# Kernel optimization log

Hardware: AMD Instinct MI355X
Metric: run time of the kernel (lower is better)

The kernel has to match this reference:

```python
import jax, jax.numpy as jnp
import numpy as np

EPS_LOG = 1e-10
DECAY = 0.99
RESET_THRESHOLD = 2


def setup_inputs() -> dict:
    key = jax.random.key(0)
    ks = jax.random.split(key, 8)
    B, C_in, T = 4, 1024, 2048
    K, D = 8192, 256
    N = B * T
    return {
        "z": jax.random.normal(ks[0], (B, C_in, T), dtype=jnp.float32),
        "u": jax.random.uniform(ks[1], (N, K), dtype=jnp.float32),
        "Wi": jax.random.normal(ks[2], (D, C_in), dtype=jnp.float32) * 0.02,
        "bi": jax.random.normal(ks[3], (D,), dtype=jnp.float32) * 0.02,
        "Wo": jax.random.normal(ks[4], (C_in, D), dtype=jnp.float32) * 0.02,
        "bo": jax.random.normal(ks[5], (C_in,), dtype=jnp.float32) * 0.02,
        "embedding": jax.random.normal(ks[6], (K, D), dtype=jnp.float32),
        "cluster_size": jnp.zeros((K,), dtype=jnp.float32),
    }


def reference(z, u, Wi, bi, Wo, bo, embedding, cluster_size):
    B, _, T = z.shape
    K, D = embedding.shape
    N = B * T

    # inproj: Conv1d with kernel_size=1 == pointwise linear over channel dim
    z_e = jnp.einsum('bit,di->bdt', z, Wi) + bi[None, :, None]  # (B, D, T)
    z_d = z_e.transpose(0, 2, 1).reshape(N, D)                   # (b t) d

    # squared-euclidean distances via norm expansion
    dist = ((z_d ** 2).sum(axis=1, keepdims=True)
            - 2.0 * (z_d @ embedding.T)
            + (embedding ** 2).sum(axis=1))                      # (N, K)

    # gumbel noise (training=True), softmax_temp = 1.0
    gumbel = -jnp.log(-jnp.log(u + EPS_LOG) + EPS_LOG)
    logits = -dist + gumbel
    y_soft = jax.nn.softmax(logits, axis=-1)                     # (N, K)

    z_q_flat = y_soft @ embedding                                # (N, D)

    # kl_div(log(avg+eps), uniform target of shape (N,K), reduction='sum')
    avg_probs = y_soft.mean(axis=0)                              # (K,)
    inv_k = 1.0 / K
    kl_loss = N * jnp.sum(inv_k * (jnp.log(inv_k) - jnp.log(avg_probs + EPS_LOG)))

    indices = jnp.argmax(y_soft, axis=1)                         # (N,) int

    z_q = z_q_flat.reshape(B, T, D).transpose(0, 2, 1)           # (B, D, T)
    vq_loss = jnp.mean((z_e - jax.lax.stop_gradient(z_q)) ** 2)

    # outproj: Conv1d kernel_size=1
    out = jnp.einsum('bdt,od->bot', z_q, Wo) + bo[None, :, None]  # (B, C_in, T)

    # box_result: active_num uses cluster_size BEFORE the EMA update
    active_num = (cluster_size > RESET_THRESHOLD).sum().astype(z.dtype)
    counts = jnp.zeros((K,), z.dtype).at[indices].add(1.0)       # one-hot column sums
    probs = counts / N                                           # == mean(one_hot, axis=0)
    perplexity = jnp.exp(-jnp.sum(probs * jnp.log(probs + EPS_LOG)))
    new_cluster_size = cluster_size * DECAY + counts * (1.0 - DECAY)

    return out, vq_loss, kl_loss, perplexity, active_num, new_cluster_size
```

## Files before the change

kernel.cpp:

```cpp
#include <hip/hip_runtime.h>
#include <hip/hip_fp16.h>


#define NROWS 8192
#define KCL   8192
#define DDIM  256
#define CIN   1024
#define TSEQ  2048
#define EPSL  1e-10f
#define MHAT  (-140.0f)

#define OUT_SC   (4*CIN*TSEQ)

#define ZD_OFF   0
#define ZQ_OFF   (NROWS*DDIM)
#define E2_OFF   (2*NROWS*DDIM)
#define CS_OFF   (E2_OFF + KCL)
#define CNT_OFF  (CS_OFF + KCL)
#define VQ_OFF   (CNT_OFF + KCL)
#define LINV_OFF (VQ_OFF + 4)

#define ZD2W   0
#define ZQ2W   2097152
#define EBW    4194304
#define ETW    5242880
#define WOBW   6291456
#define ZFW    6422528
#define E2W    7471104
#define C2W    7479296
#define LINVW  7487488
#define CSUMW  7495680
#define CNTW   7503872
#define VQW    7512064
#define PW     7512128
#define ENDW   (PW + 33554432)

using short8v = __attribute__((ext_vector_type(8))) short;
using f32x16  = __attribute__((ext_vector_type(16))) float;

__device__ __forceinline__ ushort f2bf(float f) {
  unsigned int x = __float_as_uint(f);
  return (ushort)((x + 0x7FFFu + ((x >> 16) & 1u)) >> 16);
}
__device__ __forceinline__ float bf2f(ushort h) {
  return __uint_as_float(((unsigned int)h) << 16);
}
__device__ __forceinline__ short8v pack8(float4 a, float4 b) {
  short8v v;
  v[0] = (short)f2bf(a.x); v[1] = (short)f2bf(a.y);
  v[2] = (short)f2bf(a.z); v[3] = (short)f2bf(a.w);
  v[4] = (short)f2bf(b.x); v[5] = (short)f2bf(b.y);
  v[6] = (short)f2bf(b.z); v[7] = (short)f2bf(b.w);
  return v;
}
__device__ __forceinline__ void gload16(const void* g, void* l) {
  __builtin_amdgcn_global_load_lds(
      (const __attribute__((address_space(1))) unsigned int*)g,
      (__attribute__((address_space(3))) unsigned int*)l, 16, 0, 0);
}


__global__ __launch_bounds__(256) void e2_kernel(const float* __restrict__ E,
                                                 float* __restrict__ e2) {
  const int tid = threadIdx.x;
  const int k = blockIdx.x * 64 + (tid >> 2);
  const int p = tid & 3;
  const float* row = E + (size_t)k * DDIM + p * 64;
  float s = 0.f;
#pragma unroll
  for (int j = 0; j < 16; ++j) {
    const float4 v = *reinterpret_cast<const float4*>(row + j * 4);
    s += v.x * v.x + v.y * v.y + v.z * v.z + v.w * v.w;
  }
  s += __shfl_xor(s, 1);
  s += __shfl_xor(s, 2);
  if (p == 0) e2[k] = s;
}

__global__ __launch_bounds__(256) void e2c2_kernel(const float* __restrict__ E,
                                                   float* __restrict__ e2,
                                                   float* __restrict__ c2) {
  const int tid = threadIdx.x;
  const int k = blockIdx.x * 64 + (tid >> 2);
  const int p = tid & 3;
  const float* row = E + (size_t)k * DDIM + p * 64;
  float s = 0.f;
#pragma unroll
  for (int j = 0; j < 16; ++j) {
    const float4 v = *reinterpret_cast<const float4*>(row + j * 4);
    s += v.x * v.x + v.y * v.y + v.z * v.z + v.w * v.w;
  }
  s += __shfl_xor(s, 1);
  s += __shfl_xor(s, 2);
  if (p == 0) { e2[k] = s; c2[k] = -s - MHAT; }
}

__global__ __launch_bounds__(256) void cvteb_kernel(const float* __restrict__ E,
                                                    ushort* __restrict__ Eb) {
  const size_t i = ((size_t)blockIdx.x * 256 + threadIdx.x) * 8;
  const float4 a = *reinterpret_cast<const float4*>(E + i);
  const float4 b = *reinterpret_cast<const float4*>(E + i + 4);
  *reinterpret_cast<short8v*>(Eb + i) = pack8(a, b);
}

__global__ __launch_bounds__(256) void cvtwob_kernel(const float* __restrict__ W,
                                                     ushort* __restrict__ Wb) {
  const size_t i = ((size_t)blockIdx.x * 256 + threadIdx.x) * 8;
  const float4 a = *reinterpret_cast<const float4*>(W + i);
  const float4 b = *reinterpret_cast<const float4*>(W + i + 4);
  *reinterpret_cast<short8v*>(Wb + i) = pack8(a, b);
}

__global__ __launch_bounds__(256) void etprep_kernel(const float* __restrict__ E,
                                                     ushort* __restrict__ ET) {
  __shared__ float tb[64 * 68];
  const int t = threadIdx.x;
  const int kb = (blockIdx.x & 127) * 64;
  const int db = (blockIdx.x >> 7) * 64;
#pragma unroll
  for (int it = 0; it < 4; ++it) {
    const int r = (t >> 4) + it * 16;
    const int c = (t & 15) * 4;
    const float4 v = *reinterpret_cast<const float4*>(E + (size_t)(kb + r) * DDIM + db + c);
    tb[r * 68 + c] = v.x; tb[r * 68 + c + 1] = v.y;
    tb[r * 68 + c + 2] = v.z; tb[r * 68 + c + 3] = v.w;
  }
  __syncthreads();
  const int dl = t >> 2, kg = (t & 3) * 16;
  short8v o0, o1;
#pragma unroll
  for (int j = 0; j < 8; ++j) o0[j] = (short)f2bf(tb[(kg + j) * 68 + dl]);
#pragma unroll
  for (int j = 0; j < 8; ++j) o1[j] = (short)f2bf(tb[(kg + 8 + j) * 68 + dl]);
  ushort* dst = ET + (size_t)(db + dl) * KCL + kb + kg;
  *reinterpret_cast<short8v*>(dst) = o0;
  *reinterpret_cast<short8v*>(dst + 8) = o1;
}

__global__ __launch_bounds__(256) void cvtzf_kernel(const float* __restrict__ zd,
                                                    ushort* __restrict__ zf) {
  const int t = threadIdx.x;
  const int g = blockIdx.x;
  const int lane = t & 63, row = lane & 31, half = lane >> 5;
  const float* zr = zd + (size_t)(g * 32 + row) * DDIM + half * 8;
  ushort* dst = zf + ((size_t)g * 16 * 64 + lane) * 8;
#pragma unroll
  for (int i = 0; i < 4; ++i) {
    const int ks = (t >> 6) * 4 + i;
    const float4 a = *reinterpret_cast<const float4*>(zr + ks * 16);
    const float4 b = *reinterpret_cast<const float4*>(zr + ks * 16 + 4);
    *reinterpret_cast<short8v*>(dst + (size_t)ks * 64 * 8) = pack8(a, b);
  }
}

__global__ __launch_bounds__(256) void inproj_kernel(const float* __restrict__ z,
                                                     const float* __restrict__ Wi,
                                                     const float* __restrict__ bi,
                                                     float* __restrict__ zd) {
  __shared__ float wi_s[32 * 260];
  __shared__ float zc[32 * 64];
  const int tid = threadIdx.x;
  const int n0 = blockIdx.x * 64;
  const int b = n0 / TSEQ;
  const int t0 = n0 % TSEQ;
  const float* zb = z + (size_t)b * CIN * TSEQ;

  const int dg = tid & 63;
  const int d0 = dg * 4;
  const int wv = tid >> 6;
  const int r0 = wv * 16;

  float acc[4][16];
#pragma unroll
  for (int c = 0; c < 4; ++c)
#pragma unroll
    for (int r = 0; r < 16; ++r) acc[c][r] = 0.f;

  for (int i0 = 0; i0 < CIN; i0 += 32) {
    __syncthreads();
    {
      const int iiq = (tid & 7) * 4;
      const int dt = tid >> 3;
#pragma unroll
      for (int p = 0; p < 8; ++p) {
        const int d = dt + p * 32;
        const float4 w = *reinterpret_cast<const float4*>(Wi + (size_t)d * CIN + i0 + iiq);
        wi_s[(iiq + 0) * 260 + d] = w.x;
        wi_s[(iiq + 1) * 260 + d] = w.y;
        wi_s[(iiq + 2) * 260 + d] = w.z;
        wi_s[(iiq + 3) * 260 + d] = w.w;
      }
      const int rr = tid & 63;
      const int iib = tid >> 6;
#pragma unroll
      for (int p = 0; p < 8; ++p) {
        const int ii = iib + p * 4;
        zc[ii * 64 + rr] = zb[(size_t)(i0 + ii) * TSEQ + t0 + rr];
      }
    }
    __syncthreads();
#pragma unroll
    for (int ii = 0; ii < 32; ++ii) {
      const float4 w = *reinterpret_cast<const float4*>(&wi_s[ii * 260 + d0]);
#pragma unroll
      for (int rq = 0; rq < 4; ++rq) {
        const float4 zv = *reinterpret_cast<const float4*>(&zc[ii * 64 + r0 + rq * 4]);
        const float zz[4] = {zv.x, zv.y, zv.z, zv.w};
#pragma unroll
        for (int q = 0; q < 4; ++q) {
          acc[0][rq * 4 + q] += w.x * zz[q];
          acc[1][rq * 4 + q] += w.y * zz[q];
          acc[2][rq * 4 + q] += w.z * zz[q];
          acc[3][rq * 4 + q] += w.w * zz[q];
        }
      }
    }
  }
  const float4 bv = *reinterpret_cast<const float4*>(bi + d0);
#pragma unroll
  for (int r = 0; r < 16; ++r) {
    float4 o;
    o.x = acc[0][r] + bv.x;
    o.y = acc[1][r] + bv.y;
    o.z = acc[2][r] + bv.z;
    o.w = acc[3][r] + bv.w;
    *reinterpret_cast<float4*>(zd + (size_t)(n0 + r0 + r) * DDIM + d0) = o;
  }
}

__global__ __launch_bounds__(512, 4) void flash3_kernel(
    const ushort* __restrict__ ZF, const float* __restrict__ u,
    const ushort* __restrict__ Eb, const float* __restrict__ c2,
    ushort* __restrict__ P) {
  __shared__ ushort Es[2 * 32 * 256];
  __shared__ ushort Ps[256 * 32];
  const int tid = threadIdx.x;
  const int l = tid & 63, w = tid >> 6;
  const int half = l >> 5;
  const int nb = blockIdx.x & 31, kq = blockIdx.x >> 5;
  const int n0 = nb * 256;
  const int kbase = kq * 512;

  short8v A[16];
  {
    const ushort* zf = ZF + ((size_t)(nb * 8 + w) * 16 * 64 + l) * 8;
#pragma unroll
    for (int ks = 0; ks < 16; ++ks)
      A[ks] = *reinterpret_cast<const short8v*>(zf + (size_t)ks * 512);
  }

  {
#pragma unroll
    for (int pp = 0; pp < 2; ++pp) {
      const int q = tid + pp * 512, r = q >> 5, c = q & 31;
      gload16(Eb + (size_t)(kbase + r) * 256 + (size_t)(c ^ (r & 7)) * 8, &Es[q * 8]);
    }
  }

  const int rowu = n0 + w * 32 + 4 * half;
  const float* ubase = u + ((size_t)rowu << 13);
  const int r31 = l & 31;

  for (int kt = 0; kt < 16; ++kt) {
    const int cur = kt & 1;
    const int k0 = kbase + kt * 32;
    const int col = k0 + r31;

    float upre[16];
    {
      const float* ub = ubase + col;
#pragma unroll
      for (int reg = 0; reg < 16; ++reg) {
        const int dr = (reg & 3) + 8 * (reg >> 2);
        upre[reg] = ub[(size_t)dr << 13];
      }
    }
    const float ce = c2[col];

    __syncthreads();

    if (kt < 15) {
      const int k0n = k0 + 32;
#pragma unroll
      for (int pp = 0; pp < 2; ++pp) {
        const int q = tid + pp * 512, r = q >> 5, c = q & 31;
        gload16(Eb + (size_t)(k0n + r) * 256 + (size_t)(c ^ (r & 7)) * 8,
                &Es[(cur ^ 1) * 8192 + q * 8]);
      }
    }

    const ushort* Ecur = Es + cur * 8192;
    f32x16 acc;
#pragma unroll
    for (int i = 0; i < 16; ++i) acc[i] = 0.f;
#pragma unroll
    for (int ks = 0; ks < 16; ++ks) {
      const int cc = (ks * 2 + half) ^ (r31 & 7);
      const short8v B = *reinterpret_cast<const short8v*>(Ecur + r31 * 256 + cc * 8);
      acc = __builtin_amdgcn_mfma_f32_32x32x16_bf16(A[ks], B, acc, 0, 0, 0);
    }

    {
      ushort* psr = Ps + (w * 32 + 4 * half) * 32 + r31;
#pragma unroll
      for (int reg = 0; reg < 16; ++reg) {
        const int dr = (reg & 3) + 8 * (reg >> 2);
        const float D = 1e-10f - __logf(upre[reg] + 1e-10f);
        const float pe = __fdividef(__expf(fmaf(acc[reg], 2.f, ce)), D);
        psr[dr * 32] = f2bf(pe);
      }
    }
    asm volatile("s_waitcnt lgkmcnt(0)" ::: "memory");
    __builtin_amdgcn_sched_barrier(0);
    {
      const int fr = w * 32 + (l >> 1), part = l & 1;
      const ushort* src = Ps + fr * 32 + part * 16;
      ushort* dst = P + (size_t)(n0 + fr) * KCL + k0 + part * 16;
      *reinterpret_cast<short8v*>(dst) = *reinterpret_cast<const short8v*>(src);
      *reinterpret_cast<short8v*>(dst + 8) = *reinterpret_cast<const short8v*>(src + 8);
    }
  }
}

__global__ __launch_bounds__(256) void rowpass_kernel(
    const ushort* __restrict__ P, const float* __restrict__ zd,
    const float* __restrict__ E, const float* __restrict__ e2,
    const float* __restrict__ u, float* __restrict__ linv,
    float* __restrict__ counts) {
  const int l = threadIdx.x & 63;
  const int w = threadIdx.x >> 6;
  const int n = blockIdx.x * 4 + w;
  const ushort* pr = P + (size_t)n * KCL;
  float lsum = 0.f;
  float bv[4] = {-1.f, -1.f, -1.f, -1.f};
  int bi[4] = {0x7fffffff, 0x7fffffff, 0x7fffffff, 0x7fffffff};
  for (int it = 0; it < 16; ++it) {
    const short8v v = *reinterpret_cast<const short8v*>(pr + it * 512 + l * 8);
#pragma unroll
    for (int j = 0; j < 8; ++j) {
      const float f = bf2f((ushort)v[j]);
      lsum += f;
      const int kk = it * 512 + l * 8 + j;
      const bool c0 = f > bv[0], c1 = f > bv[1], c2 = f > bv[2], c3 = f > bv[3];
      const float n3 = c2 ? bv[2] : f; const int i3 = c2 ? bi[2] : kk;
      const float n2 = c1 ? bv[1] : f; const int i2 = c1 ? bi[1] : kk;
      const float n1 = c0 ? bv[0] : f; const int i1 = c0 ? bi[0] : kk;
      bv[3] = c3 ? n3 : bv[3]; bi[3] = c3 ? i3 : bi[3];
      bv[2] = c2 ? n2 : bv[2]; bi[2] = c2 ? i2 : bi[2];
      bv[1] = c1 ? n1 : bv[1]; bi[1] = c1 ? i1 : bi[1];
      bv[0] = c0 ? f : bv[0];  bi[0] = c0 ? kk : bi[0];
    }
  }
#pragma unroll
  for (int mk = 1; mk < 64; mk <<= 1) {
    lsum += __shfl_xor(lsum, mk);
    float ov[4]; int oi[4];
#pragma unroll
    for (int i = 0; i < 4; ++i) { ov[i] = __shfl_xor(bv[i], mk); oi[i] = __shfl_xor(bi[i], mk); }
#pragma unroll
    for (int i = 0; i < 4; ++i) {
      const float f = ov[i]; const int kk = oi[i];
      const bool c0 = (f > bv[0]) || (f == bv[0] && kk < bi[0]);
      const bool c1 = (f > bv[1]) || (f == bv[1] && kk < bi[1]);
      const bool c2 = (f > bv[2]) || (f == bv[2] && kk < bi[2]);
      const bool c3 = (f > bv[3]) || (f == bv[3] && kk < bi[3]);
      const float n3 = c2 ? bv[2] : f; const int i3 = c2 ? bi[2] : kk;
      const float n2 = c1 ? bv[1] : f; const int i2 = c1 ? bi[1] : kk;
      const float n1 = c0 ? bv[0] : f; const int i1 = c0 ? bi[0] : kk;
      bv[3] = c3 ? n3 : bv[3]; bi[3] = c3 ? i3 : bi[3];
      bv[2] = c2 ? n2 : bv[2]; bi[2] = c2 ? i2 : bi[2];
      bv[1] = c1 ? n1 : bv[1]; bi[1] = c1 ? i1 : bi[1];
      bv[0] = c0 ? f : bv[0];  bi[0] = c0 ? kk : bi[0];
    }
  }
  const float4 zv = *reinterpret_cast<const float4*>(zd + (size_t)n * DDIM + l * 4);
  float best = -1e30f; int besti = 0x7fffffff;
#pragma unroll
  for (int c = 0; c < 4; ++c) {
    const int kc = bi[c];
    const float4 ev = *reinterpret_cast<const float4*>(E + (size_t)kc * DDIM + l * 4);
    float d = zv.x * ev.x + zv.y * ev.y + zv.z * ev.z + zv.w * ev.w;
#pragma unroll
    for (int mk = 1; mk < 64; mk <<= 1) d += __shfl_xor(d, mk);
    const float uu = u[(size_t)n * KCL + kc];
    const float D = 1e-10f - __logf(uu + 1e-10f);
    const float g = -__logf(D);
    const float lg = 2.f * d - e2[kc] + g;
    if (lg > best || (lg == best && kc < besti)) { best = lg; besti = kc; }
  }
  if (l == 0) {
    atomicAdd(&counts[besti], 1.f);
    linv[n] = 1.f / lsum;
  }
}

__global__ __launch_bounds__(256) void colsum2_kernel(const ushort* __restrict__ P,
                                                      const float* __restrict__ linv,
                                                      float* __restrict__ colsum) {
  __shared__ float cs[512];
  const int t = threadIdx.x;
  cs[t] = 0.f; cs[t + 256] = 0.f;
  __syncthreads();
  const int kb = blockIdx.x & 15;
  const int nb = blockIdx.x >> 4;
  const int k0 = kb * 512 + (t & 63) * 8;
  const int r0 = nb * 256 + (t >> 6);
  float a[8] = {0.f, 0.f, 0.f, 0.f, 0.f, 0.f, 0.f, 0.f};
  for (int i = 0; i < 64; ++i) {
    const int n = r0 + i * 4;
    const float lv = linv[n];
    const short8v v = *reinterpret_cast<const short8v*>(P + (size_t)n * KCL + k0);
#pragma unroll
    for (int j = 0; j < 8; ++j) a[j] += bf2f((ushort)v[j]) * lv;
  }
#pragma unroll
  for (int j = 0; j < 8; ++j) atomicAdd(&cs[(t & 63) * 8 + j], a[j]);
  __syncthreads();
  atomicAdd(&colsum[kb * 512 + t], cs[t]);
  atomicAdd(&colsum[kb * 512 + t + 256], cs[t + 256]);
}

__global__ __launch_bounds__(512, 2) void pv_kernel(
    const ushort* __restrict__ P, const ushort* __restrict__ ET,
    float* __restrict__ parts) {
  __shared__ ushort ps[128 * 64];
  __shared__ ushort es[256 * 64];
  const int tid = threadIdx.x;
  const int l = tid & 63, w = tid >> 6;
  const int half = l >> 5;
  const int nb = blockIdx.x & 63, ks = blockIdx.x >> 6;
  const int n0 = nb * 128;
  const int kc0 = ks * 2048;
  const int nw = w & 1, dw = w >> 1;

  f32x16 acc00, acc01, acc10, acc11;
#pragma unroll
  for (int i = 0; i < 16; ++i) { acc00[i] = 0.f; acc01[i] = 0.f; acc10[i] = 0.f; acc11[i] = 0.f; }

  short8v rp[2], re[4];
  {
#pragma unroll
    for (int pp = 0; pp < 2; ++pp) {
      const int q = tid * 2 + pp; const int r = q >> 3, c = q & 7;
      rp[pp] = *reinterpret_cast<const short8v*>(P + (size_t)(n0 + r) * KCL + kc0 + c * 8);
    }
#pragma unroll
    for (int pp = 0; pp < 4; ++pp) {
      const int q = tid * 4 + pp; const int r = q >> 3, c = q & 7;
      re[pp] = *reinterpret_cast<const short8v*>(ET + (size_t)r * KCL + kc0 + c * 8);
    }
  }
  for (int t = 0; t < 32; ++t) {
#pragma unroll
    for (int pp = 0; pp < 2; ++pp) {
      const int q = tid * 2 + pp; const int r = q >> 3, c = q & 7;
      *reinterpret_cast<short8v*>(ps + r * 64 + ((c ^ (r & 7))) * 8) = rp[pp];
    }
#pragma unroll
    for (int pp = 0; pp < 4; ++pp) {
      const int q = tid * 4 + pp; const int r = q >> 3, c = q & 7;
      *reinterpret_cast<short8v*>(es + r * 64 + ((c ^ (r & 7))) * 8) = re[pp];
    }
    __syncthreads();
    if (t < 31) {
      const int kc = kc0 + (t + 1) * 64;
#pragma unroll
      for (int pp = 0; pp < 2; ++pp) {
        const int q = tid * 2 + pp; const int r = q >> 3, c = q & 7;
        rp[pp] = *reinterpret_cast<const short8v*>(P + (size_t)(n0 + r) * KCL + kc + c * 8);
      }
#pragma unroll
      for (int pp = 0; pp < 4; ++pp) {
        const int q = tid * 4 + pp; const int r = q >> 3, c = q & 7;
        re[pp] = *reinterpret_cast<const short8v*>(ET + (size_t)r * KCL + kc + c * 8);
      }
    }
#pragma unroll
    for (int ksn = 0; ksn < 4; ++ksn) {
      const int cc = ksn * 2 + half;
      short8v a0, a1, b0, b1;
      { const int r = nw * 64 + (l & 31);      a0 = *reinterpret_cast<const short8v*>(ps + r * 64 + ((cc ^ (r & 7))) * 8); }
      { const int r = nw * 64 + 32 + (l & 31); a1 = *reinterpret_cast<const short8v*>(ps + r * 64 + ((cc ^ (r & 7))) * 8); }
      { const int r = dw * 64 + (l & 31);      b0 = *reinterpret_cast<const short8v*>(es + r * 64 + ((cc ^ (r & 7))) * 8); }
      { const int r = dw * 64 + 32 + (l & 31); b1 = *reinterpret_cast<const short8v*>(es + r * 64 + ((cc ^ (r & 7))) * 8); }
      acc00 = __builtin_amdgcn_mfma_f32_32x32x16_bf16(a0, b0, acc00, 0, 0, 0);
      acc01 = __builtin_amdgcn_mfma_f32_32x32x16_bf16(a0, b1, acc01, 0, 0, 0);
      acc10 = __builtin_amdgcn_mfma_f32_32x32x16_bf16(a1, b0, acc10, 0, 0, 0);
      acc11 = __builtin_amdgcn_mfma_f32_32x32x16_bf16(a1, b1, acc11, 0, 0, 0);
    }
    __syncthreads();
  }
  float* pbase = parts + (size_t)ks * NROWS * DDIM;
#pragma unroll
  for (int reg = 0; reg < 16; ++reg) {
    const int dr = (reg & 3) + 8 * (reg >> 2) + 4 * half;
    {
      const int nloc = nw * 64 + dr;
      float* zr = pbase + (size_t)(n0 + nloc) * DDIM + dw * 64 + (l & 31);
      zr[0]  = acc00[reg];
      zr[32] = acc01[reg];
    }
    {
      const int nloc = nw * 64 + 32 + dr;
      float* zr = pbase + (size_t)(n0 + nloc) * DDIM + dw * 64 + (l & 31);
      zr[0]  = acc10[reg];
      zr[32] = acc11[reg];
    }
  }
}

__global__ __launch_bounds__(256) void zqred_kernel(const float* __restrict__ parts,
                                                    const float* __restrict__ linv,
                                                    const float* __restrict__ zd,
                                                    float* __restrict__ zq,
                                                    float* __restrict__ vqs) {
  const size_t i = ((size_t)blockIdx.x * 256 + threadIdx.x) * 8;
  const int n = (int)(i >> 8);
  const float lv = linv[n];
  float s = 0.f;
#pragma unroll
  for (int j = 0; j < 8; j += 4) {
    float4 p0 = *reinterpret_cast<const float4*>(parts + i + j);
    const float4 p1 = *reinterpret_cast<const float4*>(parts + i + j + (size_t)NROWS * DDIM);
    const float4 p2 = *reinterpret_cast<const float4*>(parts + i + j + (size_t)2 * NROWS * DDIM);
    const float4 p3 = *reinterpret_cast<const float4*>(parts + i + j + (size_t)3 * NROWS * DDIM);
    const float4 a = *reinterpret_cast<const float4*>(zd + i + j);
    float4 o;
    o.x = (p0.x + p1.x + p2.x + p3.x) * lv;
    o.y = (p0.y + p1.y + p2.y + p3.y) * lv;
    o.z = (p0.z + p1.z + p2.z + p3.z) * lv;
    o.w = (p0.w + p1.w + p2.w + p3.w) * lv;
    *reinterpret_cast<float4*>(zq + i + j) = o;
    const float dx = a.x - o.x, dy = a.y - o.y, dz = a.z - o.z, dw = a.w - o.w;
    s += dx * dx + dy * dy + dz * dz + dw * dw;
  }
#pragma unroll
  for (int mk = 1; mk < 64; mk <<= 1) s += __shfl_xor(s, mk);
  if ((threadIdx.x & 63) == 0) atomicAdd(vqs, s);
}

__global__ __launch_bounds__(256) void outproj2_kernel(const float* __restrict__ zq,
                                                       const ushort* __restrict__ Wob,
                                                       const float* __restrict__ bo,
                                                       float* __restrict__ outp) {
  extern __shared__ char smem[];
  ushort* zs = (ushort*)smem;
  ushort* wsld = zs + 64 * 256;
  const int tid = threadIdx.x;
  const int l = tid & 63, w = tid >> 6;
  const int half = l >> 5;
  const int nb = blockIdx.x >> 4, ob = blockIdx.x & 15;
  const int n0 = nb * 64, o0 = ob * 64;
  const int nw = w & 1, ow = w >> 1;
  {
    const int row = tid >> 2, seg = tid & 3;
    const float* zr = zq + (size_t)(n0 + row) * DDIM + seg * 64;
    const ushort* wr = Wob + (size_t)(o0 + row) * DDIM + seg * 64;
#pragma unroll
    for (int g = 0; g < 8; ++g) {
      const float4 a = *reinterpret_cast<const float4*>(zr + g * 8);
      const float4 b = *reinterpret_cast<const float4*>(zr + g * 8 + 4);
      const int c = seg * 8 + g;
      *reinterpret_cast<short8v*>(zs + row * 256 + ((c ^ (row & 7))) * 8) = pack8(a, b);
      const short8v wv = *reinterpret_cast<const short8v*>(wr + g * 8);
      *reinterpret_cast<short8v*>(wsld + row * 256 + ((c ^ (row & 7))) * 8) = wv;
    }
  }
  __syncthreads();
  f32x16 acc;
#pragma unroll
  for (int i = 0; i < 16; ++i) acc[i] = 0.f;
#pragma unroll
  for (int ksn = 0; ksn < 16; ++ksn) {
    const int cc = ksn * 2 + half;
    const int ra = nw * 32 + (l & 31);
    const int rb = ow * 32 + (l & 31);
    const short8v a = *reinterpret_cast<const short8v*>(zs + ra * 256 + ((cc ^ (ra & 7))) * 8);
    const short8v b = *reinterpret_cast<const short8v*>(wsld + rb * 256 + ((cc ^ (rb & 7))) * 8);
    acc = __builtin_amdgcn_mfma_f32_32x32x16_bf16(a, b, acc, 0, 0, 0);
  }
  const int o = o0 + ow * 32 + (l & 31);
  const float bv = bo[o];
  const int nbase = n0 + nw * 32 + 4 * half;
#pragma unroll
  for (int rq = 0; rq < 4; ++rq) {
    const int n = nbase + rq * 8;
    const int b = n >> 11;
    const int tt = n & 2047;
    float4 ov;
    ov.x = acc[rq * 4 + 0] + bv;
    ov.y = acc[rq * 4 + 1] + bv;
    ov.z = acc[rq * 4 + 2] + bv;
    ov.w = acc[rq * 4 + 3] + bv;
    *reinterpret_cast<float4*>(outp + ((size_t)b * CIN + o) * TSEQ + tt) = ov;
  }
}

template <bool STORE_LG>
__global__ __launch_bounds__(512) void flash_kernel(
    const float* __restrict__ zd, const float* __restrict__ u,
    const float* __restrict__ E, const float* __restrict__ e2g,
    float* __restrict__ zq, float* __restrict__ colsum,
    float* __restrict__ counts, float* __restrict__ vqsum,
    float* __restrict__ linvg, __half* __restrict__ lgbuf) {
  extern __shared__ float lds[];
  float* zs = lds;
  float* es = zs + 32 * 260;
  float* e2t = es + 64 * 260;
  float* cst = e2t + 64;
  float* red = cst + 64;

  const int tid = threadIdx.x;
  const int lane = tid & 63;
  const int wv = tid >> 6;
  const int r = (lane >> 4) & 3;
  const int kg = lane & 15;
  const int row = wv * 4 + r;
  const int n0 = blockIdx.x * 32;
  const int n = n0 + row;

  {
    const int rr = tid >> 4;
    const int iq = tid & 15;
#pragma unroll
    for (int p = 0; p < 4; ++p) {
      const int i = iq * 16 + p * 4;
      *reinterpret_cast<float4*>(&zs[rr * 260 + i]) =
          *reinterpret_cast<const float4*>(zd + (size_t)(n0 + rr) * DDIM + i);
    }
  }

  float4 accp[4];
#pragma unroll
  for (int s = 0; s < 4; ++s) accp[s] = make_float4(0.f, 0.f, 0.f, 0.f);
  float lsum = 0.f;
  float best = -1e30f;
  int bidx = 0;

  const float* zrow = zs + row * 260;

  for (int t = 0; t < KCL / 64; ++t) {
    const int k0 = t * 64;
    __syncthreads();
    {
      const int iq = tid & 15;
#pragma unroll
      for (int pp = 0; pp < 2; ++pp) {
        const int kk = (tid >> 4) + pp * 32;
#pragma unroll
        for (int p = 0; p < 4; ++p) {
          const int i = iq * 16 + p * 4;
          *reinterpret_cast<float4*>(&es[kk * 260 + i]) =
              *reinterpret_cast<const float4*>(E + (size_t)(k0 + kk) * DDIM + i);
        }
      }
      if (tid < 64) e2t[tid] = e2g[k0 + tid];
    }
    __syncthreads();

    float acc4[4] = {0.f, 0.f, 0.f, 0.f};
#pragma unroll 4
    for (int i = 0; i < DDIM; i += 4) {
      const float4 zv = *reinterpret_cast<const float4*>(zrow + i);
#pragma unroll
      for (int jj = 0; jj < 4; ++jj) {
        const float4 ev = *reinterpret_cast<const float4*>(&es[(kg + jj * 16) * 260 + i]);
        acc4[jj] += zv.x * ev.x + zv.y * ev.y + zv.z * ev.z + zv.w * ev.w;
      }
    }

    float p4[4];
    float tmax = -1e30f;
    int tidx = 0;
#pragma unroll
    for (int jj = 0; jj < 4; ++jj) {
      const int kk = kg + jj * 16;
      const float uu = u[(size_t)n * KCL + k0 + kk];
      const float g = -__logf(-__logf(uu + EPSL) + EPSL);
      const float lt = 2.f * acc4[jj] - e2t[kk] + g - MHAT;
      const float pe = __expf(lt);
      p4[jj] = pe;
      lsum += pe;
      if (lt > tmax) { tmax = lt; tidx = k0 + kk; }
    }
#pragma unroll
    for (int mk = 1; mk <= 8; mk <<= 1) {
      const float ov = __shfl_xor(tmax, mk);
      const int oi = __shfl_xor(tidx, mk);
      if (ov > tmax || (ov == tmax && oi < tidx)) { tmax = ov; tidx = oi; }
    }
    if (tmax > best) { best = tmax; bidx = tidx; }

#pragma unroll
    for (int jj = 0; jj < 4; ++jj) {
#pragma unroll 4
      for (int q = 0; q < 16; ++q) {
        const int kk = jj * 16 + q;
        const float yv = __shfl(p4[jj], (lane & 48) | q);
        const float* erow = &es[kk * 260 + kg * 16];
#pragma unroll
        for (int s = 0; s < 4; ++s) {
          const int c = (s + kg) & 3;
          const float4 ev = *reinterpret_cast<const float4*>(erow + c * 4);
          accp[s].x += yv * ev.x;
          accp[s].y += yv * ev.y;
          accp[s].z += yv * ev.z;
          accp[s].w += yv * ev.w;
        }
      }
    }
  }

#pragma unroll
  for (int mk = 1; mk <= 8; mk <<= 1) lsum += __shfl_xor(lsum, mk);
  const float linv = 1.0f / lsum;

  if (kg == 0) {
    atomicAdd(&counts[bidx], 1.0f);
    linvg[n] = linv;
  }

  float vqp = 0.f;
#pragma unroll
  for (int s = 0; s < 4; ++s) {
    const int c = (s + kg) & 3;
    const int d = kg * 16 + c * 4;
    float4 o;
    o.x = accp[s].x * linv;
    o.y = accp[s].y * linv;
    o.z = accp[s].z * linv;
    o.w = accp[s].w * linv;
    *reinterpret_cast<float4*>(zq + (size_t)n * DDIM + d) = o;
    const float4 zv = *reinterpret_cast<const float4*>(zrow + d);
    const float dx = zv.x - o.x, dy = zv.y - o.y, dz = zv.z - o.z, dw = zv.w - o.w;
    vqp += dx * dx + dy * dy + dz * dz + dw * dw;
  }
#pragma unroll
  for (int mk = 1; mk <= 32; mk <<= 1) vqp += __shfl_xor(vqp, mk);
  if (lane == 0) red[wv] = vqp;
  __syncthreads();
  if (tid == 0) {
    float s = 0.f;
#pragma unroll
    for (int ww = 0; ww < 8; ++ww) s += red[ww];
    atomicAdd(vqsum, s);
  }

  if (!STORE_LG) {
    if (tid < 64) cst[tid] = 0.f;
    for (int t = 0; t < KCL / 64; ++t) {
      const int k0 = t * 64;
      __syncthreads();
      {
        const int iq = tid & 15;
#pragma unroll
        for (int pp = 0; pp < 2; ++pp) {
          const int kk = (tid >> 4) + pp * 32;
#pragma unroll
          for (int p = 0; p < 4; ++p) {
            const int i = iq * 16 + p * 4;
            *reinterpret_cast<float4*>(&es[kk * 260 + i]) =
                *reinterpret_cast<const float4*>(E + (size_t)(k0 + kk) * DDIM + i);
          }
        }
        if (tid < 64) e2t[tid] = e2g[k0 + tid];
      }
      __syncthreads();
      float acc4[4] = {0.f, 0.f, 0.f, 0.f};
#pragma unroll 4
      for (int i = 0; i < DDIM; i += 4) {
        const float4 zv = *reinterpret_cast<const float4*>(zrow + i);
#pragma unroll
        for (int jj = 0; jj < 4; ++jj) {
          const float4 ev = *reinterpret_cast<const float4*>(&es[(kg + jj * 16) * 260 + i]);
          acc4[jj] += zv.x * ev.x + zv.y * ev.y + zv.z * ev.z + zv.w * ev.w;
        }
      }
      float cs4[4];
#pragma unroll
      for (int jj = 0; jj < 4; ++jj) {
        const int kk = kg + jj * 16;
        const float uu = u[(size_t)n * KCL + k0 + kk];
        const float g = -__logf(-__logf(uu + EPSL) + EPSL);
        const float lt = 2.f * acc4[jj] - e2t[kk] + g - MHAT;
        cs4[jj] = __expf(lt) * linv;
      }
#pragma unroll
      for (int mk = 16; mk <= 32; mk <<= 1)
#pragma unroll
        for (int jj = 0; jj < 4; ++jj) cs4[jj] += __shfl_xor(cs4[jj], mk);
      if (lane < 16) {
#pragma unroll
        for (int jj = 0; jj < 4; ++jj) atomicAdd(&cst[kg + jj * 16], cs4[jj]);
      }
      __syncthreads();
      if (tid < 64) {
        atomicAdd(&colsum[k0 + tid], cst[tid]);
        cst[tid] = 0.f;
      }
    }
  }
}

__global__ __launch_bounds__(256) void outproj_kernel(const float* __restrict__ zq,
                                                      const float* __restrict__ Wo,
                                                      const float* __restrict__ bo,
                                                      float* __restrict__ outp) {
  __shared__ float wo_s[32 * 260];
  __shared__ float zc[32 * 68];
  const int tid = threadIdx.x;
  const int n0 = (blockIdx.x >> 2) * 64;
  const int ot = (blockIdx.x & 3) * 256;
  const int b = n0 / TSEQ;
  const int t0 = n0 % TSEQ;

  const int og = tid & 63;
  const int o0 = og * 4;
  const int wv = tid >> 6;
  const int r0 = wv * 16;

  float acc[4][16];
#pragma unroll
  for (int c = 0; c < 4; ++c)
#pragma unroll
    for (int r = 0; r < 16; ++r) acc[c][r] = 0.f;

  for (int dd = 0; dd < DDIM; dd += 32) {
    __syncthreads();
    {
      const int ccq = (tid & 7) * 4;
      const int oq = tid >> 3;
#pragma unroll
      for (int p = 0; p < 8; ++p) {
        const int oo = oq + p * 32;
        const float4 w = *reinterpret_cast<const float4*>(Wo + (size_t)(ot + oo) * DDIM + dd + ccq);
        wo_s[(ccq + 0) * 260 + oo] = w.x;
        wo_s[(ccq + 1) * 260 + oo] = w.y;
        wo_s[(ccq + 2) * 260 + oo] = w.z;
        wo_s[(ccq + 3) * 260 + oo] = w.w;
      }
#pragma unroll
      for (int p = 0; p < 2; ++p) {
        const int rr = oq + p * 32;
        const float4 v = *reinterpret_cast<const float4*>(zq + (size_t)(n0 + rr) * DDIM + dd + ccq);
        zc[(ccq + 0) * 68 + rr] = v.x;
        zc[(ccq + 1) * 68 + rr] = v.y;
        zc[(ccq + 2) * 68 + rr] = v.z;
        zc[(ccq + 3) * 68 + rr] = v.w;
      }
    }
    __syncthreads();
#pragma unroll
    for (int cc = 0; cc < 32; ++cc) {
      const float4 w = *reinterpret_cast<const float4*>(&wo_s[cc * 260 + o0]);
#pragma unroll
      for (int rq = 0; rq < 4; ++rq) {
        const float4 zv = *reinterpret_cast<const float4*>(&zc[cc * 68 + r0 + rq * 4]);
        const float zz[4] = {zv.x, zv.y, zv.z, zv.w};
#pragma unroll
        for (int q = 0; q < 4; ++q) {
          acc[0][rq * 4 + q] += w.x * zz[q];
          acc[1][rq * 4 + q] += w.y * zz[q];
          acc[2][rq * 4 + q] += w.z * zz[q];
          acc[3][rq * 4 + q] += w.w * zz[q];
        }
      }
    }
  }
  const float4 bv = *reinterpret_cast<const float4*>(bo + ot + o0);
  float* ob = outp + (size_t)b * CIN * TSEQ + t0;
  const float bb[4] = {bv.x, bv.y, bv.z, bv.w};
#pragma unroll
  for (int c = 0; c < 4; ++c) {
#pragma unroll
    for (int rq = 0; rq < 4; ++rq) {
      float4 o;
      o.x = acc[c][rq * 4 + 0] + bb[c];
      o.y = acc[c][rq * 4 + 1] + bb[c];
      o.z = acc[c][rq * 4 + 2] + bb[c];
      o.w = acc[c][rq * 4 + 3] + bb[c];
      *reinterpret_cast<float4*>(ob + (size_t)(ot + o0 + c) * TSEQ + r0 + rq * 4) = o;
    }
  }
}

__global__ __launch_bounds__(256) void finalize_kernel(
    const float* __restrict__ colsum, const float* __restrict__ counts,
    const float* __restrict__ vqsum, const float* __restrict__ csin,
    float* __restrict__ outsc, float* __restrict__ ncs) {
  __shared__ float rS[3][4];
  const int tid = threadIdx.x;
  const int lane = tid & 63;
  const int wv = tid >> 6;
  float sLog = 0.f, sH = 0.f, sAct = 0.f;
  for (int k = tid; k < KCL; k += 256) {
    const float avg = colsum[k] * (1.0f / NROWS);
    sLog += __logf(avg + EPSL);
    const float pb = counts[k] * (1.0f / NROWS);
    sH += pb * __logf(pb + EPSL);
    sAct += (csin[k] > 2.0f) ? 1.f : 0.f;
    ncs[k] = csin[k] * 0.99f + counts[k] * 0.01f;
  }
#pragma unroll
  for (int mk = 1; mk <= 32; mk <<= 1) {
    sLog += __shfl_xor(sLog, mk);
    sH += __shfl_xor(sH, mk);
    sAct += __shfl_xor(sAct, mk);
  }
  if (lane == 0) { rS[0][wv] = sLog; rS[1][wv] = sH; rS[2][wv] = sAct; }
  __syncthreads();
  if (tid == 0) {
    float SL = 0.f, SH = 0.f, SA = 0.f;
#pragma unroll
    for (int w = 0; w < 4; ++w) { SL += rS[0][w]; SH += rS[1][w]; SA += rS[2][w]; }
    outsc[0] = vqsum[0] * (1.0f / ((float)NROWS * (float)DDIM));
    outsc[1] = (float)NROWS * __logf(1.0f / (float)KCL) - SL;
    outsc[2] = __expf(-SH);
    outsc[3] = SA;
  }
}

extern "C" void kernel_launch(void* const* d_in, const int* in_sizes, int n_in,
                              void* d_out, int out_size, void* d_ws, size_t ws_size,
                              hipStream_t stream) {
  (void)in_sizes; (void)n_in; (void)out_size;
  const float* z = (const float*)d_in[0];
  const float* u = (const float*)d_in[1];
  const float* Wi = (const float*)d_in[2];
  const float* bi = (const float*)d_in[3];
  const float* Wo = (const float*)d_in[4];
  const float* bo = (const float*)d_in[5];
  const float* E = (const float*)d_in[6];
  const float* csin = (const float*)d_in[7];
  float* outp = (float*)d_out;
  float* ws = (float*)d_ws;

  const size_t needNew = (size_t)ENDW * 4;
  if (ws_size >= needNew) {
    ushort* EB = (ushort*)(ws + EBW);
    ushort* ET = (ushort*)(ws + ETW);
    ushort* WOB = (ushort*)(ws + WOBW);
    ushort* ZF = (ushort*)(ws + ZFW);
    ushort* P = (ushort*)(ws + PW);

    hipMemsetAsync((void*)(ws + CSUMW), 0, (size_t)(2 * KCL + 64) * 4, stream);

    e2c2_kernel<<<KCL / 64, 256, 0, stream>>>(E, ws + E2W, ws + C2W);
    cvteb_kernel<<<1024, 256, 0, stream>>>(E, EB);
    etprep_kernel<<<512, 256, 0, stream>>>(E, ET);
    cvtwob_kernel<<<128, 256, 0, stream>>>(Wo, WOB);
    inproj_kernel<<<NROWS / 64, 256, 0, stream>>>(z, Wi, bi, ws + ZD2W);
    cvtzf_kernel<<<NROWS / 32, 256, 0, stream>>>(ws + ZD2W, ZF);

    flash3_kernel<<<512, 512, 0, stream>>>(ZF, u, EB, ws + C2W, P);
    rowpass_kernel<<<NROWS / 4, 256, 0, stream>>>(P, ws + ZD2W, E, ws + E2W, u,
                                                  ws + LINVW, ws + CNTW);
    colsum2_kernel<<<512, 256, 0, stream>>>(P, ws + LINVW, ws + CSUMW);
    pv_kernel<<<256, 512, 0, stream>>>(P, ET, outp);
    zqred_kernel<<<1024, 256, 0, stream>>>(outp, ws + LINVW, ws + ZD2W,
                                           ws + ZQ2W, ws + VQW);

    hipFuncSetAttribute(reinterpret_cast<const void*>(&outproj2_kernel),
                        hipFuncAttributeMaxDynamicSharedMemorySize, 65536);
    outproj2_kernel<<<2048, 256, 65536, stream>>>(ws + ZQ2W, WOB, bo, outp);
    finalize_kernel<<<1, 256, 0, stream>>>(ws + CSUMW, ws + CNTW, ws + VQW,
                                           csin, outp + OUT_SC, outp + OUT_SC + 4);
  } else {
    hipMemsetAsync((void*)(ws + CS_OFF), 0, (size_t)(2 * KCL + 1) * sizeof(float), stream);
    e2_kernel<<<KCL / 64, 256, 0, stream>>>(E, ws + E2_OFF);
    inproj_kernel<<<NROWS / 64, 256, 0, stream>>>(z, Wi, bi, ws + ZD_OFF);
    const int ldsB = (32 * 260 + 64 * 260 + 64 + 64 + 16) * 4;
    hipFuncSetAttribute(reinterpret_cast<const void*>(&flash_kernel<false>),
                        hipFuncAttributeMaxDynamicSharedMemorySize, ldsB);
    flash_kernel<false><<<NROWS / 32, 512, ldsB, stream>>>(
        ws + ZD_OFF, u, E, ws + E2_OFF, ws + ZQ_OFF, ws + CS_OFF, ws + CNT_OFF,
        ws + VQ_OFF, ws + LINV_OFF, (__half*)nullptr);
    outproj_kernel<<<(NROWS / 64) * 4, 256, 0, stream>>>(ws + ZQ_OFF, Wo, bo, outp);
    finalize_kernel<<<1, 256, 0, stream>>>(ws + CS_OFF, ws + CNT_OFF, ws + VQ_OFF,
                                           csin, outp + OUT_SC, outp + OUT_SC + 4);
  }
}
```

Before: 551.4 us.

## Prefetch gumbel noise one tile ahead, drop LDS staging, fuse bf16 conversion, shrink PV tile

The flash kernel now loads the next tile's u values into alternating register arrays while computing the current tile. It also writes P directly to global memory instead of staging through LDS, and its launch bound drops to 2 blocks per SM. The separate embedding bf16 conversion kernel is folded into the transpose-prep kernel. The PV kernel uses 64-row tiles with twice as many blocks for more parallelism. The risks are uncoalesced 2-byte strided P stores and higher register pressure.

```diff
diff --git a/kernel.cpp b/kernel.cpp
--- a/kernel.cpp
+++ b/kernel.cpp
@@ -36,6 +36,7 @@
 #define ENDW   (PW + 33554432)
 
 using short8v = __attribute__((ext_vector_type(8))) short;
+using short4v = __attribute__((ext_vector_type(4))) short;
 using f32x16  = __attribute__((ext_vector_type(16))) float;
 
 __device__ __forceinline__ ushort f2bf(float f) {
@@ -95,14 +96,6 @@
   if (p == 0) { e2[k] = s; c2[k] = -s - MHAT; }
 }
 
-__global__ __launch_bounds__(256) void cvteb_kernel(const float* __restrict__ E,
-                                                    ushort* __restrict__ Eb) {
-  const size_t i = ((size_t)blockIdx.x * 256 + threadIdx.x) * 8;
-  const float4 a = *reinterpret_cast<const float4*>(E + i);
-  const float4 b = *reinterpret_cast<const float4*>(E + i + 4);
-  *reinterpret_cast<short8v*>(Eb + i) = pack8(a, b);
-}
-
 __global__ __launch_bounds__(256) void cvtwob_kernel(const float* __restrict__ W,
                                                      ushort* __restrict__ Wb) {
   const size_t i = ((size_t)blockIdx.x * 256 + threadIdx.x) * 8;
@@ -112,7 +105,8 @@
 }
 
 __global__ __launch_bounds__(256) void etprep_kernel(const float* __restrict__ E,
-                                                     ushort* __restrict__ ET) {
+                                                     ushort* __restrict__ ET,
+                                                     ushort* __restrict__ EB) {
   __shared__ float tb[64 * 68];
   const int t = threadIdx.x;
   const int kb = (blockIdx.x & 127) * 64;
@@ -124,6 +118,10 @@
     const float4 v = *reinterpret_cast<const float4*>(E + (size_t)(kb + r) * DDIM + db + c);
     tb[r * 68 + c] = v.x; tb[r * 68 + c + 1] = v.y;
     tb[r * 68 + c + 2] = v.z; tb[r * 68 + c + 3] = v.w;
+    short4v o;
+    o[0] = (short)f2bf(v.x); o[1] = (short)f2bf(v.y);
+    o[2] = (short)f2bf(v.z); o[3] = (short)f2bf(v.w);
+    *reinterpret_cast<short4v*>(EB + (size_t)(kb + r) * DDIM + db + c) = o;
   }
   __syncthreads();
   const int dl = t >> 2, kg = (t & 3) * 16;
@@ -228,18 +226,58 @@
   }
 }
 
-__global__ __launch_bounds__(512, 4) void flash3_kernel(
+#define FSTEP(KT, CUR, UC, UN)                                                 \
+  {                                                                            \
+    const int k0 = kbase + (KT) * 32;                                          \
+    __syncthreads();            \
+    if ((KT) < 15) {                                                           \
+      _Pragma("unroll")                                                        \
+      for (int pp = 0; pp < 2; ++pp) {                                         \
+        const int q = tid + pp * 512, r = q >> 5, c = q & 31;                  \
+        gload16(Eb + (size_t)(k0 + 32 + r) * 256 + (size_t)(c ^ (r & 7)) * 8,  \
+                &Es[(1 - (CUR)) * 8192 + q * 8]);                              \
+      }                                                                        \
+      const float* ubn = ubase + k0 + 32 + r31;                                \
+      _Pragma("unroll")                                                        \
+      for (int reg = 0; reg < 16; ++reg) {                                     \
+        const int dr = (reg & 3) + 8 * (reg >> 2);                             \
+        UN[reg] = ubn[(size_t)dr << 13];                                       \
+      }                                                                        \
+    }                                                                          \
+    const float ce = c2[k0 + r31];                                             \
+    const ushort* Ecur = Es + (CUR) * 8192;                                    \
+    f32x16 acc;                                                                \
+    _Pragma("unroll")                                                          \
+    for (int i = 0; i < 16; ++i) acc[i] = 0.f;                                 \
+    _Pragma("unroll")                                                          \
+    for (int ks = 0; ks < 16; ++ks) {                                          \
+      const int cc = (ks * 2 + half) ^ (r31 & 7);                              \
+      const short8v B =                                                        \
+          *reinterpret_cast<const short8v*>(Ecur + r31 * 256 + cc * 8);        \
+      acc = __builtin_amdgcn_mfma_f32_32x32x16_bf16(A[ks], B, acc, 0, 0, 0);   \
+    }                                                                          \
+    ushort* pdst = P + (size_t)rowu * KCL + k0 + r31;                          \
+    _Pragma("unroll")                                                          \
+    for (int reg = 0; reg < 16; ++reg) {                                       \
+      const int dr = (reg & 3) + 8 * (reg >> 2);                               \
+      const float D = 1e-10f - __logf(UC[reg] + 1e-10f);                       \
+      const float pe = __fdividef(__expf(fmaf(acc[reg], 2.f, ce)), D);         \
+      pdst[(size_t)dr << 13] = f2bf(pe);                                       \
+    }                                                                          \
+  }
+
+__global__ __launch_bounds__(512, 2) void flash4_kernel(
     const ushort* __restrict__ ZF, const float* __restrict__ u,
     const ushort* __restrict__ Eb, const float* __restrict__ c2,
     ushort* __restrict__ P) {
   __shared__ ushort Es[2 * 32 * 256];
-  __shared__ ushort Ps[256 * 32];
   const int tid = threadIdx.x;
   const int l = tid & 63, w = tid >> 6;
   const int half = l >> 5;
   const int nb = blockIdx.x & 31, kq = blockIdx.x >> 5;
   const int n0 = nb * 256;
   const int kbase = kq * 512;
+  const int r31 = l & 31;
 
   short8v A[16];
   {
@@ -249,76 +287,27 @@
       A[ks] = *reinterpret_cast<const short8v*>(zf + (size_t)ks * 512);
   }
 
-  {
-#pragma unroll
-    for (int pp = 0; pp < 2; ++pp) {
-      const int q = tid + pp * 512, r = q >> 5, c = q & 31;
-      gload16(Eb + (size_t)(kbase + r) * 256 + (size_t)(c ^ (r & 7)) * 8, &Es[q * 8]);
-    }
-  }
-
   const int rowu = n0 + w * 32 + 4 * half;
   const float* ubase = u + ((size_t)rowu << 13);
-  const int r31 = l & 31;
-
-  for (int kt = 0; kt < 16; ++kt) {
-    const int cur = kt & 1;
-    const int k0 = kbase + kt * 32;
-    const int col = k0 + r31;
-
-    float upre[16];
-    {
-      const float* ub = ubase + col;
-#pragma unroll
-      for (int reg = 0; reg < 16; ++reg) {
-        const int dr = (reg & 3) + 8 * (reg >> 2);
-        upre[reg] = ub[(size_t)dr << 13];
-      }
-    }
-    const float ce = c2[col];
-
-    __syncthreads();
-
-    if (kt < 15) {
-      const int k0n = k0 + 32;
-#pragma unroll
-      for (int pp = 0; pp < 2; ++pp) {
-        const int q = tid + pp * 512, r = q >> 5, c = q & 31;
-        gload16(Eb + (size_t)(k0n + r) * 256 + (size_t)(c ^ (r & 7)) * 8,
-                &Es[(cur ^ 1) * 8192 + q * 8]);
-      }
-    }
-
-    const ushort* Ecur = Es + cur * 8192;
-    f32x16 acc;
-#pragma unroll
-    for (int i = 0; i < 16; ++i) acc[i] = 0.f;
-#pragma unroll
-    for (int ks = 0; ks < 16; ++ks) {
-      const int cc = (ks * 2 + half) ^ (r31 & 7);
-      const short8v B = *reinterpret_cast<const short8v*>(Ecur + r31 * 256 + cc * 8);
-      acc = __builtin_amdgcn_mfma_f32_32x32x16_bf16(A[ks], B, acc, 0, 0, 0);
-    }
-
-    {
-      ushort* psr = Ps + (w * 32 + 4 * half) * 32 + r31;
-#pragma unroll
-      for (int reg = 0; reg < 16; ++reg) {
-        const int dr = (reg & 3) + 8 * (reg >> 2);
-        const float D = 1e-10f - __logf(upre[reg] + 1e-10f);
-        const float pe = __fdividef(__expf(fmaf(acc[reg], 2.f, ce)), D);
-        psr[dr * 32] = f2bf(pe);
-      }
-    }
-    asm volatile("s_waitcnt lgkmcnt(0)" ::: "memory");
-    __builtin_amdgcn_sched_barrier(0);
-    {
-      const int fr = w * 32 + (l >> 1), part = l & 1;
-      const ushort* src = Ps + fr * 32 + part * 16;
-      ushort* dst = P + (size_t)(n0 + fr) * KCL + k0 + part * 16;
-      *reinterpret_cast<short8v*>(dst) = *reinterpret_cast<const short8v*>(src);
-      *reinterpret_cast<short8v*>(dst + 8) = *reinterpret_cast<const short8v*>(src + 8);
-    }
+
+#pragma unroll
+  for (int pp = 0; pp < 2; ++pp) {
+    const int q = tid + pp * 512, r = q >> 5, c = q & 31;
+    gload16(Eb + (size_t)(kbase + r) * 256 + (size_t)(c ^ (r & 7)) * 8, &Es[q * 8]);
+  }
+  float uA[16], uB[16];
+  {
+    const float* ub = ubase + kbase + r31;
+#pragma unroll
+    for (int reg = 0; reg < 16; ++reg) {
+      const int dr = (reg & 3) + 8 * (reg >> 2);
+      uA[reg] = ub[(size_t)dr << 13];
+    }
+  }
+
+  for (int kt2 = 0; kt2 < 16; kt2 += 2) {
+    FSTEP(kt2, 0, uA, uB);
+    FSTEP(kt2 + 1, 1, uB, uA);
   }
 }
 
@@ -420,73 +409,66 @@
   atomicAdd(&colsum[kb * 512 + t + 256], cs[t + 256]);
 }
 
-__global__ __launch_bounds__(512, 2) void pv_kernel(
+__global__ __launch_bounds__(512, 2) void pv2_kernel(
     const ushort* __restrict__ P, const ushort* __restrict__ ET,
     float* __restrict__ parts) {
-  __shared__ ushort ps[128 * 64];
+  __shared__ ushort ps[64 * 64];
   __shared__ ushort es[256 * 64];
   const int tid = threadIdx.x;
   const int l = tid & 63, w = tid >> 6;
   const int half = l >> 5;
-  const int nb = blockIdx.x & 63, ks = blockIdx.x >> 6;
-  const int n0 = nb * 128;
+  const int r31 = l & 31;
+  const int nb = blockIdx.x & 127, ks = blockIdx.x >> 7;
+  const int n0 = nb * 64;
   const int kc0 = ks * 2048;
   const int nw = w & 1, dw = w >> 1;
 
-  f32x16 acc00, acc01, acc10, acc11;
-#pragma unroll
-  for (int i = 0; i < 16; ++i) { acc00[i] = 0.f; acc01[i] = 0.f; acc10[i] = 0.f; acc11[i] = 0.f; }
-
-  short8v rp[2], re[4];
+  f32x16 acc0, acc1;
+#pragma unroll
+  for (int i = 0; i < 16; ++i) { acc0[i] = 0.f; acc1[i] = 0.f; }
+
+  short8v rp, re[4];
   {
-#pragma unroll
-    for (int pp = 0; pp < 2; ++pp) {
-      const int q = tid * 2 + pp; const int r = q >> 3, c = q & 7;
-      rp[pp] = *reinterpret_cast<const short8v*>(P + (size_t)(n0 + r) * KCL + kc0 + c * 8);
-    }
+    const int r = tid >> 3, c = tid & 7;
+    rp = *reinterpret_cast<const short8v*>(P + (size_t)(n0 + r) * KCL + kc0 + c * 8);
 #pragma unroll
     for (int pp = 0; pp < 4; ++pp) {
-      const int q = tid * 4 + pp; const int r = q >> 3, c = q & 7;
-      re[pp] = *reinterpret_cast<const short8v*>(ET + (size_t)r * KCL + kc0 + c * 8);
+      const int q = tid * 4 + pp; const int rr = q >> 3, cc = q & 7;
+      re[pp] = *reinterpret_cast<const short8v*>(ET + (size_t)rr * KCL + kc0 + cc * 8);
     }
   }
   for (int t = 0; t < 32; ++t) {
-#pragma unroll
-    for (int pp = 0; pp < 2; ++pp) {
-      const int q = tid * 2 + pp; const int r = q >> 3, c = q & 7;
-      *reinterpret_cast<short8v*>(ps + r * 64 + ((c ^ (r & 7))) * 8) = rp[pp];
+    {
+      const int r = tid >> 3, c = tid & 7;
+      *reinterpret_cast<short8v*>(ps + r * 64 + ((c ^ (r & 7))) * 8) = rp;
     }
 #pragma unroll
     for (int pp = 0; pp < 4; ++pp) {
-      const int q = tid * 4 + pp; const int r = q >> 3, c = q & 7;
-      *reinterpret_cast<short8v*>(es + r * 64 + ((c ^ (r & 7))) * 8) = re[pp];
+      const int q = tid * 4 + pp; const int rr = q >> 3, cc = q & 7;
+      *reinterpret_cast<short8v*>(es + rr * 64 + ((cc ^ (rr & 7))) * 8) = re[pp];
     }
     __syncthreads();
     if (t < 31) {
       const int kc = kc0 + (t + 1) * 64;
-#pragma unroll
-      for (int pp = 0; pp < 2; ++pp) {
-        const int q = tid * 2 + pp; const int r = q >> 3, c = q & 7;
-        rp[pp] = *reinterpret_cast<const short8v*>(P + (size_t)(n0 + r) * KCL + kc + c * 8);
+      {
+        const int r = tid >> 3, c = tid & 7;
+        rp = *reinterpret_cast<const short8v*>(P + (size_t)(n0 + r) * KCL + kc + c * 8);
       }
 #pragma unroll
       for (int pp = 0; pp < 4; ++pp) {
-        const int q = tid * 4 + pp; const int r = q >> 3, c = q & 7;
-        re[pp] = *reinterpret_cast<const short8v*>(ET + (size_t)r * KCL + kc + c * 8);
+        const int q = tid * 4 + pp; const int rr = q >> 3, cc = q & 7;
+        re[pp] = *reinterpret_cast<const short8v*>(ET + (size_t)rr * KCL + kc + cc * 8);
       }
     }
 #pragma unroll
     for (int ksn = 0; ksn < 4; ++ksn) {
       const int cc = ksn * 2 + half;
-      short8v a0, a1, b0, b1;
-      { const int r = nw * 64 + (l & 31);      a0 = *reinterpret_cast<const short8v*>(ps + r * 64 + ((cc ^ (r & 7))) * 8); }
-      { const int r = nw * 64 + 32 + (l & 31); a1 = *reinterpret_cast<const short8v*>(ps + r * 64 + ((cc ^ (r & 7))) * 8); }
-      { const int r = dw * 64 + (l & 31);      b0 = *reinterpret_cast<const short8v*>(es + r * 64 + ((cc ^ (r & 7))) * 8); }
-      { const int r = dw * 64 + 32 + (l & 31); b1 = *reinterpret_cast<const short8v*>(es + r * 64 + ((cc ^ (r & 7))) * 8); }
-      acc00 = __builtin_amdgcn_mfma_f32_32x32x16_bf16(a0, b0, acc00, 0, 0, 0);
-      acc01 = __builtin_amdgcn_mfma_f32_32x32x16_bf16(a0, b1, acc01, 0, 0, 0);
-      acc10 = __builtin_amdgcn_mfma_f32_32x32x16_bf16(a1, b0, acc10, 0, 0, 0);
-      acc11 = __builtin_amdgcn_mfma_f32_32x32x16_bf16(a1, b1, acc11, 0, 0, 0);
+      short8v a, b0, b1;
+      { const int r = nw * 32 + r31;      a  = *reinterpret_cast<const short8v*>(ps + r * 64 + ((cc ^ (r & 7))) * 8); }
+      { const int r = dw * 64 + r31;      b0 = *reinterpret_cast<const short8v*>(es + r * 64 + ((cc ^ (r & 7))) * 8); }
+      { const int r = dw * 64 + 32 + r31; b1 = *reinterpret_cast<const short8v*>(es + r * 64 + ((cc ^ (r & 7))) * 8); }
+      acc0 = __builtin_amdgcn_mfma_f32_32x32x16_bf16(a, b0, acc0, 0, 0, 0);
+      acc1 = __builtin_amdgcn_mfma_f32_32x32x16_bf16(a, b1, acc1, 0, 0, 0);
     }
     __syncthreads();
   }
@@ -494,18 +476,9 @@
 #pragma unroll
   for (int reg = 0; reg < 16; ++reg) {
     const int dr = (reg & 3) + 8 * (reg >> 2) + 4 * half;
-    {
-      const int nloc = nw * 64 + dr;
-      float* zr = pbase + (size_t)(n0 + nloc) * DDIM + dw * 64 + (l & 31);
-      zr[0]  = acc00[reg];
-      zr[32] = acc01[reg];
-    }
-    {
-      const int nloc = nw * 64 + 32 + dr;
-      float* zr = pbase + (size_t)(n0 + nloc) * DDIM + dw * 64 + (l & 31);
-      zr[0]  = acc10[reg];
-      zr[32] = acc11[reg];
-    }
+    float* zr = pbase + (size_t)(n0 + nw * 32 + dr) * DDIM + dw * 64 + r31;
+    zr[0]  = acc0[reg];
+    zr[32] = acc1[reg];
   }
 }
 
@@ -946,17 +919,16 @@
     hipMemsetAsync((void*)(ws + CSUMW), 0, (size_t)(2 * KCL + 64) * 4, stream);
 
     e2c2_kernel<<<KCL / 64, 256, 0, stream>>>(E, ws + E2W, ws + C2W);
-    cvteb_kernel<<<1024, 256, 0, stream>>>(E, EB);
-    etprep_kernel<<<512, 256, 0, stream>>>(E, ET);
+    etprep_kernel<<<512, 256, 0, stream>>>(E, ET, EB);
     cvtwob_kernel<<<128, 256, 0, stream>>>(Wo, WOB);
     inproj_kernel<<<NROWS / 64, 256, 0, stream>>>(z, Wi, bi, ws + ZD2W);
     cvtzf_kernel<<<NROWS / 32, 256, 0, stream>>>(ws + ZD2W, ZF);
 
-    flash3_kernel<<<512, 512, 0, stream>>>(ZF, u, EB, ws + C2W, P);
+    flash4_kernel<<<512, 512, 0, stream>>>(ZF, u, EB, ws + C2W, P);
     rowpass_kernel<<<NROWS / 4, 256, 0, stream>>>(P, ws + ZD2W, E, ws + E2W, u,
                                                   ws + LINVW, ws + CNTW);
     colsum2_kernel<<<512, 256, 0, stream>>>(P, ws + LINVW, ws + CSUMW);
-    pv_kernel<<<256, 512, 0, stream>>>(P, ET, outp);
+    pv2_kernel<<<512, 512, 0, stream>>>(P, ET, outp);
     zqred_kernel<<<1024, 256, 0, stream>>>(outp, ws + LINVW, ws + ZD2W,
                                            ws + ZQ2W, ws + VQW);
 
```

Result: no change. 542.6 us (-1.6%).
